# Kernel tuning notes

Hardware: AMD Instinct MI355X
Metric: run time of the kernel (lower is better)

## Reference

```python
import jax, jax.numpy as jnp
import numpy as np

N = 50000          # nodes
F = 128            # feature dim (indim = outdim)
AVG_DEG = 12       # random edges per node (plus one self-loop)
AVG_D_LOG = 2.6    # avg_d['log'] used by PNA scalers
EPS = 1e-5         # PNA std epsilon / BatchNorm eps


def setup_inputs() -> dict:
    key = jax.random.key(0)
    k1, k2, k3, k4 = jax.random.split(key, 4)
    h = jax.random.normal(k1, (N, F), dtype=jnp.float32)
    E_rand = N * AVG_DEG
    src_r = jax.random.randint(k2, (E_rand,), 0, N)
    dst_r = jax.random.randint(k3, (E_rand,), 0, N)
    loop = jnp.arange(N)
    src = jnp.concatenate([src_r, loop]).astype(jnp.int64) if jax.config.jax_enable_x64 else jnp.concatenate([src_r, loop]).astype(jnp.int32)
    dst = jnp.concatenate([dst_r, loop]).astype(src.dtype)
    concat_dim = F * (1 + 4 * 3)  # indim * (1 + n_aggr * n_scalers)
    W = jax.random.normal(k4, (concat_dim, F), dtype=jnp.float32) * (1.0 / np.sqrt(concat_dim))
    b = jnp.zeros((F,), dtype=jnp.float32)
    gamma = jnp.ones((F,), dtype=jnp.float32)
    beta = jnp.zeros((F,), dtype=jnp.float32)
    return {"h": h, "src": src, "dst": dst, "W": W, "b": b, "gamma": gamma, "beta": beta}


def _pna_forward(h, W, b, gamma, beta, src, dst):
    n = h.shape[0]
    m = h[src]                                            # [E, F] gathered mailbox
    deg = jax.ops.segment_sum(jnp.ones(src.shape[0], h.dtype), dst, num_segments=n)
    deg = jnp.maximum(deg, 1.0)[:, None]                  # every node has a self-loop
    s = jax.ops.segment_sum(m, dst, num_segments=n)
    mean = s / deg
    mx = jax.ops.segment_max(m, dst, num_segments=n)
    mn = jax.ops.segment_min(m, dst, num_segments=n)
    mean_sq = jax.ops.segment_sum(m * m, dst, num_segments=n) / deg
    std = jnp.sqrt(jax.nn.relu(mean_sq - mean * mean) + EPS)
    agg = jnp.concatenate([mean, mx, mn, std], axis=1)    # [N, 4F]
    logd = jnp.log(deg + 1.0)                             # [N, 1]
    scaled = jnp.concatenate([agg,
                              agg * (logd / AVG_D_LOG),
                              agg * (AVG_D_LOG / logd)], axis=1)  # [N, 12F]
    hc = jnp.concatenate([h, scaled], axis=1)             # [N, 13F]
    out = hc @ W + b                                      # posttrans (single linear)
    out = jax.nn.relu(out)                                # activation (dropout p=0)
    mu = out.mean(axis=0)                                 # BatchNorm1d, training stats
    var = out.var(axis=0)                                 # biased variance (torch)
    out = gamma * (out - mu) * jax.lax.rsqrt(var + EPS) + beta
    return out


def reference(h, src, dst, W, b, gamma, beta):
    return _pna_forward(h, W, b, gamma, beta, src, dst)
```

## Files before the change

kernel.cpp:

```cpp
#include <hip/hip_runtime.h>
#include <math.h>

#define FDIM 128
#define AVG_D_LOGF 2.6f
#define BN_EPS 1e-5f
#define NK 10

using f32x4 = __attribute__((ext_vector_type(4))) float;
using s16x8 = __attribute__((ext_vector_type(8))) short;
using u16x8 = __attribute__((ext_vector_type(8))) unsigned short;

__device__ __forceinline__ unsigned short f2bf(float x) {
  unsigned int u = __float_as_uint(x);
  u += 0x7FFFu + ((u >> 16) & 1u);
  return (unsigned short)(u >> 16);
}
__device__ __forceinline__ float bf2f(unsigned short u) {
  return __uint_as_float(((unsigned int)u) << 16);
}

__device__ __forceinline__ void gload16(const void* g, void* l) {
  __builtin_amdgcn_global_load_lds(
      (const __attribute__((address_space(1))) void*)g,
      (__attribute__((address_space(3))) void*)l, 16, 0, 0);
}

__global__ void prep_kernel(const float* __restrict__ h, unsigned short* __restrict__ hb,
                            const float* __restrict__ W, unsigned short* __restrict__ wBT,
                            const int* __restrict__ dst, int* __restrict__ deg,
                            int w0, int w1, int w2, int K) {
  int i = blockIdx.x * 256 + threadIdx.x;
  if (i < w0) {
    const f32x4* sp = (const f32x4*)h + (size_t)i * 2;
    f32x4 v0 = sp[0], v1 = sp[1];
    u16x8 o;
    o[0] = f2bf(v0[0]); o[1] = f2bf(v0[1]); o[2] = f2bf(v0[2]); o[3] = f2bf(v0[3]);
    o[4] = f2bf(v1[0]); o[5] = f2bf(v1[1]); o[6] = f2bf(v1[2]); o[7] = f2bf(v1[3]);
    *((u16x8*)hb + i) = o;
  } else if (i < w0 + w1) {
    int idx = i - w0;
    int k = idx >> 7, j = idx & 127;
    wBT[(size_t)j * K + k] = f2bf(W[idx]);
  } else if (i < w0 + w1 + w2) {
    atomicAdd(&deg[dst[i - w0 - w1]], 1);
  }
}

__global__ void scan1(const int* __restrict__ deg, int* __restrict__ offs,
                      int* __restrict__ bsums, int n) {
  __shared__ int tmp[256];
  int t = threadIdx.x, i = blockIdx.x * 256 + t;
  int v = (i < n) ? deg[i] : 0;
  tmp[t] = v; __syncthreads();
  for (int d = 1; d < 256; d <<= 1) {
    int x = (t >= d) ? tmp[t - d] : 0;
    __syncthreads();
    tmp[t] += x;
    __syncthreads();
  }
  if (i < n) offs[i] = tmp[t] - v;
  if (t == 255) bsums[blockIdx.x] = tmp[255];
}

__global__ void scan2(int* __restrict__ bsums, int nb) {
  __shared__ int tmp[256];
  int t = threadIdx.x;
  int v = (t < nb) ? bsums[t] : 0;
  tmp[t] = v; __syncthreads();
  for (int d = 1; d < 256; d <<= 1) {
    int x = (t >= d) ? tmp[t - d] : 0;
    __syncthreads();
    tmp[t] += x;
    __syncthreads();
  }
  if (t < nb) bsums[t] = tmp[t] - v;
}

__global__ void scan3(int* __restrict__ offs, const int* __restrict__ bsums, int n, int E) {
  int i = blockIdx.x * 256 + threadIdx.x;
  if (i < n) offs[i] += bsums[blockIdx.x];
  if (i == 0) offs[n] = E;
}

__global__ void csr_fill(const int* __restrict__ src, const int* __restrict__ dst,
                         const int* __restrict__ offs, int* __restrict__ cursor,
                         int* __restrict__ csr, int E) {
  int i = blockIdx.x * 256 + threadIdx.x;
  if (i < E) {
    int d = dst[i];
    int pos = offs[d] + atomicAdd(&cursor[d], 1);
    csr[pos] = src[i];
  }
}

__global__ __launch_bounds__(256) void agg_kernel(
    const unsigned short* __restrict__ hb, const int* __restrict__ csr,
    const int* __restrict__ offs, unsigned short* __restrict__ aggb,
    float2* __restrict__ s12a, int n) {
  const int gw = (blockIdx.x * 256 + threadIdx.x) >> 6;
  const int lane = threadIdx.x & 63;
  if (gw >= n) return;
  const int beg = offs[gw], end = offs[gw + 1];
  const unsigned int* hp = (const unsigned int*)hb;
  float s0 = 0.f, s1 = 0.f, q0 = 0.f, q1 = 0.f;
  float mx0 = -INFINITY, mx1 = -INFINITY, mn0 = INFINITY, mn1 = INFINITY;
  int e = beg;
  for (; e + 4 <= end; e += 4) {
    int i0 = csr[e], i1 = csr[e + 1], i2 = csr[e + 2], i3 = csr[e + 3];
    unsigned int a = hp[(size_t)i0 * 64 + lane];
    unsigned int b = hp[(size_t)i1 * 64 + lane];
    unsigned int c = hp[(size_t)i2 * 64 + lane];
    unsigned int d = hp[(size_t)i3 * 64 + lane];
    float a0 = bf2f((unsigned short)a), a1 = bf2f((unsigned short)(a >> 16));
    float b0 = bf2f((unsigned short)b), b1 = bf2f((unsigned short)(b >> 16));
    float c0 = bf2f((unsigned short)c), c1 = bf2f((unsigned short)(c >> 16));
    float d0 = bf2f((unsigned short)d), d1 = bf2f((unsigned short)(d >> 16));
    s0 += (a0 + b0) + (c0 + d0); s1 += (a1 + b1) + (c1 + d1);
    q0 += (a0 * a0 + b0 * b0) + (c0 * c0 + d0 * d0);
    q1 += (a1 * a1 + b1 * b1) + (c1 * c1 + d1 * d1);
    mx0 = fmaxf(fmaxf(mx0, a0), fmaxf(b0, fmaxf(c0, d0)));
    mx1 = fmaxf(fmaxf(mx1, a1), fmaxf(b1, fmaxf(c1, d1)));
    mn0 = fminf(fminf(mn0, a0), fminf(b0, fminf(c0, d0)));
    mn1 = fminf(fminf(mn1, a1), fminf(b1, fminf(c1, d1)));
  }
  for (; e < end; ++e) {
    int i0 = csr[e];
    unsigned int a = hp[(size_t)i0 * 64 + lane];
    float a0 = bf2f((unsigned short)a), a1 = bf2f((unsigned short)(a >> 16));
    s0 += a0; s1 += a1;
    q0 += a0 * a0; q1 += a1 * a1;
    mx0 = fmaxf(mx0, a0); mx1 = fmaxf(mx1, a1);
    mn0 = fminf(mn0, a0); mn1 = fminf(mn1, a1);
  }
  float degf = (float)(end - beg);
  if (degf < 1.f) degf = 1.f;
  const float inv = 1.f / degf;
  float me0 = s0 * inv, me1 = s1 * inv;
  float v0 = q0 * inv - me0 * me0, v1 = q1 * inv - me1 * me1;
  float st0 = sqrtf(fmaxf(v0, 0.f) + BN_EPS);
  float st1 = sqrtf(fmaxf(v1, 0.f) + BN_EPS);
  unsigned int base = (unsigned int)gw * 512u + (unsigned int)lane * 2u;
  *(unsigned int*)&aggb[base      ] = (unsigned int)f2bf(me0) | ((unsigned int)f2bf(me1) << 16);
  *(unsigned int*)&aggb[base + 128] = (unsigned int)f2bf(mx0) | ((unsigned int)f2bf(mx1) << 16);
  *(unsigned int*)&aggb[base + 256] = (unsigned int)f2bf(mn0) | ((unsigned int)f2bf(mn1) << 16);
  *(unsigned int*)&aggb[base + 384] = (unsigned int)f2bf(st0) | ((unsigned int)f2bf(st1) << 16);
  if (lane == 0) {
    float logd = logf(degf + 1.f);
    s12a[gw] = make_float2(logd / AVG_D_LOGF, AVG_D_LOGF / logd);
  }
}

__global__ __launch_bounds__(256, 3) void gemm_kernel(
    const unsigned short* __restrict__ hb, const unsigned short* __restrict__ wBT,
    const unsigned short* __restrict__ aggb, const float2* __restrict__ s12a,
    const float* __restrict__ bias, float* __restrict__ out,
    float* __restrict__ bnsum, float* __restrict__ bnsq, int n, int K) {
  __shared__ s16x8 As[1024];
  __shared__ s16x8 Bs[3][512];
  const int t = threadIdx.x;
  const int lane = t & 63;
  const int w = t >> 6;
  const int wr = w >> 1, wc = w & 1;
  const int hi = lane >> 4, lr = lane & 15, rx7 = lr & 7;

  const int nwg = gridDim.x;
  const int q = nwg >> 3, r = nwg & 7;
  const int xcd = blockIdx.x & 7, jj = blockIdx.x >> 3;
  const int bx = (xcd < r ? xcd * (q + 1) : r * (q + 1) + (xcd - r) * q) + jj;

  const int m0 = (bx >> 1) * 128;
  const int n0 = (bx & 1) * 64;

  f32x4 acc[3][4][2] = {};

  auto stage = [&](int ss) {
    const bool ph1 = (ss < 2);
    #pragma unroll
    for (int i = 0; i < 4; ++i) {
      int unit = w * 256 + i * 64 + lane;
      int row = unit >> 3, x = unit & 7;
      int node = m0 + row; if (node >= n) node = n - 1;
      int xo = (x ^ (row & 7)) << 3;
      const unsigned short* src = ph1
          ? hb   + (size_t)node * FDIM + ss * 64 + xo
          : aggb + (size_t)node * 512 + (ss - 2) * 64 + xo;
      gload16(src, &As[w * 256 + i * 64]);
    }
    const int nsec = ph1 ? 1 : 3;
    for (int s = 0; s < nsec; ++s) {
      int koff = ph1 ? ss * 64 : (FDIM + s * 512 + (ss - 2) * 64);
      #pragma unroll
      for (int i = 0; i < 2; ++i) {
        int unit = w * 128 + i * 64 + lane;
        int row = unit >> 3, x = unit & 7;
        const unsigned short* src =
            wBT + (size_t)(n0 + row) * K + koff + ((x ^ (row & 7)) << 3);
        gload16(src, &Bs[s][w * 128 + i * 64]);
      }
    }
  };

  for (int step = 0; step < NK; ++step) {
    stage(step);
    __syncthreads();
    #pragma unroll
    for (int ks = 0; ks < 2; ++ks) {
      s16x8 a[4];
      #pragma unroll
      for (int m = 0; m < 4; ++m) {
        int row = wr * 64 + m * 16 + lr;
        a[m] = As[row * 8 + ((ks * 4 + hi) ^ rx7)];
      }
      #pragma unroll
      for (int s = 0; s < 3; ++s) {
        if (step < 2 && s > 0) continue;
        int rb = wc * 32 + lr;
        s16x8 b0 = Bs[s][rb * 8 + ((ks * 4 + hi) ^ rx7)];
        s16x8 b1 = Bs[s][(rb + 16) * 8 + ((ks * 4 + hi) ^ rx7)];
        #pragma unroll
        for (int m = 0; m < 4; ++m) {
          acc[s][m][0] = __builtin_amdgcn_mfma_f32_16x16x32_bf16(a[m], b0, acc[s][m][0], 0, 0, 0);
          acc[s][m][1] = __builtin_amdgcn_mfma_f32_16x16x32_bf16(a[m], b1, acc[s][m][1], 0, 0, 0);
        }
      }
    }
    __syncthreads();
  }

  float* red = (float*)&As[0];
  if (t < 128) red[t] = 0.f;
  __syncthreads();

  const float bv0 = bias[n0 + wc * 32 + lr];
  const float bv1 = bias[n0 + wc * 32 + 16 + lr];
  float cs[2] = {0.f, 0.f}, cq[2] = {0.f, 0.f};
  #pragma unroll
  for (int m = 0; m < 4; ++m) {
    #pragma unroll
    for (int i = 0; i < 4; ++i) {
      int grow = m0 + wr * 64 + m * 16 + hi * 4 + i;
      if (grow >= n) continue;
      float2 sv = s12a[grow];
      #pragma unroll
      for (int nn = 0; nn < 2; ++nn) {
        float v = acc[0][m][nn][i] + sv.x * acc[1][m][nn][i] + sv.y * acc[2][m][nn][i]
                + (nn ? bv1 : bv0);
        v = fmaxf(v, 0.f);
        out[(size_t)grow * FDIM + n0 + wc * 32 + nn * 16 + lr] = v;
        cs[nn] += v; cq[nn] += v * v;
      }
    }
  }
  #pragma unroll
  for (int nn = 0; nn < 2; ++nn) {
    int lc = wc * 32 + nn * 16 + lr;
    atomicAdd(&red[lc], cs[nn]);
    atomicAdd(&red[64 + lc], cq[nn]);
  }
  __syncthreads();
  if (t < 64)       atomicAdd(&bnsum[n0 + t], red[t]);
  else if (t < 128) atomicAdd(&bnsq[n0 + t - 64], red[t]);
}

__global__ void bn_norm(float* __restrict__ out, const float* __restrict__ bnsum,
                        const float* __restrict__ bnsq, const float* __restrict__ gamma,
                        const float* __restrict__ beta, int n) {
  const int j = threadIdx.x & 127;
  const float invN = 1.f / (float)n;
  const float mu = bnsum[j] * invN;
  const float var = bnsq[j] * invN - mu * mu;
  const float rs = rsqrtf(var + BN_EPS);
  const float sc = gamma[j] * rs;
  const float sh = beta[j] - mu * sc;
  const int gt = blockIdx.x * 256 + threadIdx.x;
  const int row0 = gt >> 7;
  const int rstride = (gridDim.x * 256) >> 7;
  for (int i = row0; i < n; i += rstride) {
    size_t idx = (size_t)i * FDIM + j;
    out[idx] = out[idx] * sc + sh;
  }
}

extern "C" void kernel_launch(void* const* d_in, const int* in_sizes, int n_in,
                              void* d_out, int out_size, void* d_ws, size_t ws_size,
                              hipStream_t stream) {
  const float* h     = (const float*)d_in[0];
  const int*   src   = (const int*)d_in[1];
  const int*   dst   = (const int*)d_in[2];
  const float* W     = (const float*)d_in[3];
  const float* bias  = (const float*)d_in[4];
  const float* gamma = (const float*)d_in[5];
  const float* beta  = (const float*)d_in[6];
  float* out = (float*)d_out;

  const int n = in_sizes[0] / FDIM;
  const int E = in_sizes[1];
  const int K = in_sizes[3] / FDIM;

  char* base = (char*)d_ws;
  size_t off = 0;
  auto alloc = [&](size_t bytes) -> void* {
    void* p = base + off;
    off += (bytes + 255) & ~(size_t)255;
    return p;
  };
  int*   deg    = (int*)  alloc(4ull * n);
  int*   cursor = (int*)  alloc(4ull * n);
  float* bnsum  = (float*)alloc(512);
  float* bnsq   = (float*)alloc(512);
  const size_t zlen = off;
  int*    offs  = (int*)  alloc(4ull * (n + 1));
  int*    bsums = (int*)  alloc(4ull * 256);
  int*    csr   = (int*)  alloc(4ull * E);
  float2* s12a  = (float2*)alloc(8ull * n);
  unsigned short* aggb = (unsigned short*)alloc(2ull * (size_t)n * 512);
  unsigned short* wBT  = (unsigned short*)alloc(2ull * (size_t)K * FDIM);
  unsigned short* hb   = (unsigned short*)alloc(2ull * (size_t)n * FDIM);
  (void)ws_size; (void)n_in; (void)out_size;

  const int eb = (E + 255) / 256;
  const int nb = (n + 255) / 256;
  const int w0 = n * FDIM / 8;
  const int w1 = K * FDIM;
  const int w2 = E;

  hipMemsetAsync(d_ws, 0, zlen, stream);
  prep_kernel<<<(w0 + w1 + w2 + 255) / 256, 256, 0, stream>>>(h, hb, W, wBT, dst, deg,
                                                              w0, w1, w2, K);
  scan1<<<nb, 256, 0, stream>>>(deg, offs, bsums, n);
  scan2<<<1, 256, 0, stream>>>(bsums, nb);
  scan3<<<nb, 256, 0, stream>>>(offs, bsums, n, E);
  csr_fill<<<eb, 256, 0, stream>>>(src, dst, offs, cursor, csr, E);
  agg_kernel<<<(n + 3) / 4, 256, 0, stream>>>(hb, csr, offs, aggb, s12a, n);
  const int gblocks = ((n + 127) / 128) * 2;
  gemm_kernel<<<gblocks, 256, 0, stream>>>(hb, wBT, aggb, s12a, bias,
                                           out, bnsum, bnsq, n, K);
  bn_norm<<<1024, 256, 0, stream>>>(out, bnsum, bnsq, gamma, beta, n);
}
```

Measured before the change: 175.9 us.

## Drop LDS staging in GEMM and fold scan3 into consumers

The GEMM kernel no longer stages A and B tiles through LDS with global_load_lds and barriers. Each wave now loads its MFMA operands directly from global memory into registers, which removes the per-step __syncthreads and the LDS footprint. The third scan pass is also removed: csr_fill and agg_kernel add the block prefix sum from bsums when they read offsets. This saves a kernel launch, but operand reuse across waves now depends on L1/L2 caches instead of shared memory, so global load traffic and latency exposure rise.

Measured after the change: 226.0 us. 28.5% more time.

```diff
diff --git a/kernel.cpp b/kernel.cpp
--- a/kernel.cpp
+++ b/kernel.cpp
@@ -4,7 +4,6 @@
 #define FDIM 128
 #define AVG_D_LOGF 2.6f
 #define BN_EPS 1e-5f
-#define NK 10
 
 using f32x4 = __attribute__((ext_vector_type(4))) float;
 using s16x8 = __attribute__((ext_vector_type(8))) short;
@@ -17,12 +16,6 @@
 }
 __device__ __forceinline__ float bf2f(unsigned short u) {
   return __uint_as_float(((unsigned int)u) << 16);
-}
-
-__device__ __forceinline__ void gload16(const void* g, void* l) {
-  __builtin_amdgcn_global_load_lds(
-      (const __attribute__((address_space(1))) void*)g,
-      (__attribute__((address_space(3))) void*)l, 16, 0, 0);
 }
 
 __global__ void prep_kernel(const float* __restrict__ h, unsigned short* __restrict__ hb,
@@ -76,31 +69,26 @@
   if (t < nb) bsums[t] = tmp[t] - v;
 }
 
-__global__ void scan3(int* __restrict__ offs, const int* __restrict__ bsums, int n, int E) {
-  int i = blockIdx.x * 256 + threadIdx.x;
-  if (i < n) offs[i] += bsums[blockIdx.x];
-  if (i == 0) offs[n] = E;
-}
-
 __global__ void csr_fill(const int* __restrict__ src, const int* __restrict__ dst,
-                         const int* __restrict__ offs, int* __restrict__ cursor,
-                         int* __restrict__ csr, int E) {
+                         const int* __restrict__ offs, const int* __restrict__ bsums,
+                         int* __restrict__ cursor, int* __restrict__ csr, int E) {
   int i = blockIdx.x * 256 + threadIdx.x;
   if (i < E) {
     int d = dst[i];
-    int pos = offs[d] + atomicAdd(&cursor[d], 1);
+    int pos = offs[d] + bsums[d >> 8] + atomicAdd(&cursor[d], 1);
     csr[pos] = src[i];
   }
 }
 
 __global__ __launch_bounds__(256) void agg_kernel(
     const unsigned short* __restrict__ hb, const int* __restrict__ csr,
-    const int* __restrict__ offs, unsigned short* __restrict__ aggb,
-    float2* __restrict__ s12a, int n) {
+    const int* __restrict__ offs, const int* __restrict__ bsums,
+    unsigned short* __restrict__ aggb, float2* __restrict__ s12a, int n, int E) {
   const int gw = (blockIdx.x * 256 + threadIdx.x) >> 6;
   const int lane = threadIdx.x & 63;
   if (gw >= n) return;
-  const int beg = offs[gw], end = offs[gw + 1];
+  const int beg = offs[gw] + bsums[gw >> 8];
+  const int end = (gw + 1 < n) ? offs[gw + 1] + bsums[(gw + 1) >> 8] : E;
   const unsigned int* hp = (const unsigned int*)hb;
   float s0 = 0.f, s1 = 0.f, q0 = 0.f, q1 = 0.f;
   float mx0 = -INFINITY, mx1 = -INFINITY, mn0 = INFINITY, mn1 = INFINITY;
@@ -150,18 +138,17 @@
   }
 }
 
-__global__ __launch_bounds__(256, 3) void gemm_kernel(
+__global__ __launch_bounds__(256) void gemm_kernel(
     const unsigned short* __restrict__ hb, const unsigned short* __restrict__ wBT,
     const unsigned short* __restrict__ aggb, const float2* __restrict__ s12a,
     const float* __restrict__ bias, float* __restrict__ out,
     float* __restrict__ bnsum, float* __restrict__ bnsq, int n, int K) {
-  __shared__ s16x8 As[1024];
-  __shared__ s16x8 Bs[3][512];
+  __shared__ float red[128];
   const int t = threadIdx.x;
   const int lane = t & 63;
   const int w = t >> 6;
   const int wr = w >> 1, wc = w & 1;
-  const int hi = lane >> 4, lr = lane & 15, rx7 = lr & 7;
+  const int hi = lane >> 4, lr = lane & 15;
 
   const int nwg = gridDim.x;
   const int q = nwg >> 3, r = nwg & 7;
@@ -173,61 +160,68 @@
 
   f32x4 acc[3][4][2] = {};
 
-  auto stage = [&](int ss) {
-    const bool ph1 = (ss < 2);
-    #pragma unroll
-    for (int i = 0; i < 4; ++i) {
-      int unit = w * 256 + i * 64 + lane;
-      int row = unit >> 3, x = unit & 7;
-      int node = m0 + row; if (node >= n) node = n - 1;
-      int xo = (x ^ (row & 7)) << 3;
-      const unsigned short* src = ph1
-          ? hb   + (size_t)node * FDIM + ss * 64 + xo
-          : aggb + (size_t)node * 512 + (ss - 2) * 64 + xo;
-      gload16(src, &As[w * 256 + i * 64]);
+  const unsigned short* aH[4];
+  const unsigned short* aG[4];
+  #pragma unroll
+  for (int m = 0; m < 4; ++m) {
+    int row = m0 + wr * 64 + m * 16 + lr;
+    if (row >= n) row = n - 1;
+    aH[m] = hb   + (size_t)row * FDIM + hi * 8;
+    aG[m] = aggb + (size_t)row * 512  + hi * 8;
+  }
+  const unsigned short* bP[2];
+  #pragma unroll
+  for (int nn = 0; nn < 2; ++nn)
+    bP[nn] = wBT + (size_t)(n0 + wc * 32 + nn * 16 + lr) * K + hi * 8;
+
+  #pragma unroll
+  for (int step = 0; step < 2; ++step) {
+    const int kg = step * 64;
+    s16x8 a[2][4], b[2][2];
+    #pragma unroll
+    for (int ks = 0; ks < 2; ++ks) {
+      #pragma unroll
+      for (int m = 0; m < 4; ++m) a[ks][m] = *(const s16x8*)(aH[m] + kg + ks * 32);
+      #pragma unroll
+      for (int nn = 0; nn < 2; ++nn) b[ks][nn] = *(const s16x8*)(bP[nn] + kg + ks * 32);
     }
-    const int nsec = ph1 ? 1 : 3;
-    for (int s = 0; s < nsec; ++s) {
-      int koff = ph1 ? ss * 64 : (FDIM + s * 512 + (ss - 2) * 64);
-      #pragma unroll
-      for (int i = 0; i < 2; ++i) {
-        int unit = w * 128 + i * 64 + lane;
-        int row = unit >> 3, x = unit & 7;
-        const unsigned short* src =
-            wBT + (size_t)(n0 + row) * K + koff + ((x ^ (row & 7)) << 3);
-        gload16(src, &Bs[s][w * 128 + i * 64]);
-      }
+    #pragma unroll
+    for (int ks = 0; ks < 2; ++ks)
+      #pragma unroll
+      for (int m = 0; m < 4; ++m)
+        #pragma unroll
+        for (int nn = 0; nn < 2; ++nn)
+          acc[0][m][nn] = __builtin_amdgcn_mfma_f32_16x16x32_bf16(a[ks][m], b[ks][nn],
+                                                                  acc[0][m][nn], 0, 0, 0);
+  }
+
+  for (int step = 0; step < 8; ++step) {
+    const int kg = step * 64;
+    s16x8 a[2][4];
+    #pragma unroll
+    for (int ks = 0; ks < 2; ++ks)
+      #pragma unroll
+      for (int m = 0; m < 4; ++m) a[ks][m] = *(const s16x8*)(aG[m] + kg + ks * 32);
+    #pragma unroll
+    for (int s = 0; s < 3; ++s) {
+      const int koff = FDIM + s * 512 + kg;
+      s16x8 b[2][2];
+      #pragma unroll
+      for (int ks = 0; ks < 2; ++ks)
+        #pragma unroll
+        for (int nn = 0; nn < 2; ++nn)
+          b[ks][nn] = *(const s16x8*)(bP[nn] + koff + ks * 32);
+      #pragma unroll
+      for (int ks = 0; ks < 2; ++ks)
+        #pragma unroll
+        for (int m = 0; m < 4; ++m)
+          #pragma unroll
+          for (int nn = 0; nn < 2; ++nn)
+            acc[s][m][nn] = __builtin_amdgcn_mfma_f32_16x16x32_bf16(a[ks][m], b[ks][nn],
+                                                                    acc[s][m][nn], 0, 0, 0);
     }
-  };
-
-  for (int step = 0; step < NK; ++step) {
-    stage(step);
-    __syncthreads();
-    #pragma unroll
-    for (int ks = 0; ks < 2; ++ks) {
-      s16x8 a[4];
-      #pragma unroll
-      for (int m = 0; m < 4; ++m) {
-        int row = wr * 64 + m * 16 + lr;
-        a[m] = As[row * 8 + ((ks * 4 + hi) ^ rx7)];
-      }
-      #pragma unroll
-      for (int s = 0; s < 3; ++s) {
-        if (step < 2 && s > 0) continue;
-        int rb = wc * 32 + lr;
-        s16x8 b0 = Bs[s][rb * 8 + ((ks * 4 + hi) ^ rx7)];
-        s16x8 b1 = Bs[s][(rb + 16) * 8 + ((ks * 4 + hi) ^ rx7)];
-        #pragma unroll
-        for (int m = 0; m < 4; ++m) {
-          acc[s][m][0] = __builtin_amdgcn_mfma_f32_16x16x32_bf16(a[m], b0, acc[s][m][0], 0, 0, 0);
-          acc[s][m][1] = __builtin_amdgcn_mfma_f32_16x16x32_bf16(a[m], b1, acc[s][m][1], 0, 0, 0);
-        }
-      }
-    }
-    __syncthreads();
-  }
-
-  float* red = (float*)&As[0];
+  }
+
   if (t < 128) red[t] = 0.f;
   __syncthreads();
 
@@ -329,9 +323,8 @@
                                                               w0, w1, w2, K);
   scan1<<<nb, 256, 0, stream>>>(deg, offs, bsums, n);
   scan2<<<1, 256, 0, stream>>>(bsums, nb);
-  scan3<<<nb, 256, 0, stream>>>(offs, bsums, n, E);
-  csr_fill<<<eb, 256, 0, stream>>>(src, dst, offs, cursor, csr, E);
-  agg_kernel<<<(n + 3) / 4, 256, 0, stream>>>(hb, csr, offs, aggb, s12a, n);
+  csr_fill<<<eb, 256, 0, stream>>>(src, dst, offs, bsums, cursor, csr, E);
+  agg_kernel<<<(n + 3) / 4, 256, 0, stream>>>(hb, csr, offs, bsums, aggb, s12a, n, E);
   const int gblocks = ((n + 127) / 128) * 2;
   gemm_kernel<<<gblocks, 256, 0, stream>>>(hb, wBT, aggb, s12a, bias,
                                            out, bnsum, bnsq, n, K);
```

## Fold block-sum scan into consumers and split edges across half-waves in aggregation

Applied to the files above, without the earlier changes.

Removes the scan2/scan3 launches by having csr_fill and agg_kernel each redo the small block-sum prefix scan in shared memory and add it to the partial offsets. The aggregation kernel now has each half-wave handle alternate edges with 8-byte loads per lane, then combines the halves with cross-lane shuffles before writing. This cuts two launches and doubles the gathers in flight per edge step, at the cost of repeating the block-sum scan in every block and adding shuffle reductions.

New measurement: 184.1 us. 4.7% more time.

```diff
diff --git a/kernel.cpp b/kernel.cpp
--- a/kernel.cpp
+++ b/kernel.cpp
@@ -62,88 +62,127 @@
   if (t == 255) bsums[blockIdx.x] = tmp[255];
 }
 
-__global__ void scan2(int* __restrict__ bsums, int nb) {
+__global__ void csr_fill(const int* __restrict__ src, const int* __restrict__ dst,
+                         const int* __restrict__ offs, const int* __restrict__ bsums,
+                         int* __restrict__ cursor, int* __restrict__ csr, int E, int nb) {
   __shared__ int tmp[256];
-  int t = threadIdx.x;
-  int v = (t < nb) ? bsums[t] : 0;
-  tmp[t] = v; __syncthreads();
-  for (int d = 1; d < 256; d <<= 1) {
-    int x = (t >= d) ? tmp[t - d] : 0;
-    __syncthreads();
-    tmp[t] += x;
-    __syncthreads();
-  }
-  if (t < nb) bsums[t] = tmp[t] - v;
-}
-
-__global__ void scan3(int* __restrict__ offs, const int* __restrict__ bsums, int n, int E) {
-  int i = blockIdx.x * 256 + threadIdx.x;
-  if (i < n) offs[i] += bsums[blockIdx.x];
-  if (i == 0) offs[n] = E;
-}
-
-__global__ void csr_fill(const int* __restrict__ src, const int* __restrict__ dst,
-                         const int* __restrict__ offs, int* __restrict__ cursor,
-                         int* __restrict__ csr, int E) {
-  int i = blockIdx.x * 256 + threadIdx.x;
+  __shared__ int ex[256];
+  const int t = threadIdx.x;
+  {
+    int v = (t < nb) ? bsums[t] : 0;
+    tmp[t] = v; __syncthreads();
+    for (int d = 1; d < 256; d <<= 1) {
+      int x = (t >= d) ? tmp[t - d] : 0;
+      __syncthreads();
+      tmp[t] += x;
+      __syncthreads();
+    }
+    ex[t] = tmp[t] - v;
+    __syncthreads();
+  }
+  int i = blockIdx.x * 256 + t;
   if (i < E) {
     int d = dst[i];
-    int pos = offs[d] + atomicAdd(&cursor[d], 1);
+    int pos = offs[d] + ex[d >> 8] + atomicAdd(&cursor[d], 1);
     csr[pos] = src[i];
   }
 }
 
 __global__ __launch_bounds__(256) void agg_kernel(
     const unsigned short* __restrict__ hb, const int* __restrict__ csr,
-    const int* __restrict__ offs, unsigned short* __restrict__ aggb,
-    float2* __restrict__ s12a, int n) {
+    const int* __restrict__ offs, const int* __restrict__ bsums,
+    unsigned short* __restrict__ aggb, float2* __restrict__ s12a,
+    int n, int E, int nb) {
+  __shared__ int tmp[256];
+  __shared__ int ex[256];
+  {
+    int t = threadIdx.x;
+    int v = (t < nb) ? bsums[t] : 0;
+    tmp[t] = v; __syncthreads();
+    for (int d = 1; d < 256; d <<= 1) {
+      int x = (t >= d) ? tmp[t - d] : 0;
+      __syncthreads();
+      tmp[t] += x;
+      __syncthreads();
+    }
+    ex[t] = tmp[t] - v;
+    __syncthreads();
+  }
   const int gw = (blockIdx.x * 256 + threadIdx.x) >> 6;
   const int lane = threadIdx.x & 63;
   if (gw >= n) return;
-  const int beg = offs[gw], end = offs[gw + 1];
-  const unsigned int* hp = (const unsigned int*)hb;
-  float s0 = 0.f, s1 = 0.f, q0 = 0.f, q1 = 0.f;
-  float mx0 = -INFINITY, mx1 = -INFINITY, mn0 = INFINITY, mn1 = INFINITY;
-  int e = beg;
-  for (; e + 4 <= end; e += 4) {
-    int i0 = csr[e], i1 = csr[e + 1], i2 = csr[e + 2], i3 = csr[e + 3];
-    unsigned int a = hp[(size_t)i0 * 64 + lane];
-    unsigned int b = hp[(size_t)i1 * 64 + lane];
-    unsigned int c = hp[(size_t)i2 * 64 + lane];
-    unsigned int d = hp[(size_t)i3 * 64 + lane];
-    float a0 = bf2f((unsigned short)a), a1 = bf2f((unsigned short)(a >> 16));
-    float b0 = bf2f((unsigned short)b), b1 = bf2f((unsigned short)(b >> 16));
-    float c0 = bf2f((unsigned short)c), c1 = bf2f((unsigned short)(c >> 16));
-    float d0 = bf2f((unsigned short)d), d1 = bf2f((unsigned short)(d >> 16));
-    s0 += (a0 + b0) + (c0 + d0); s1 += (a1 + b1) + (c1 + d1);
-    q0 += (a0 * a0 + b0 * b0) + (c0 * c0 + d0 * d0);
-    q1 += (a1 * a1 + b1 * b1) + (c1 * c1 + d1 * d1);
-    mx0 = fmaxf(fmaxf(mx0, a0), fmaxf(b0, fmaxf(c0, d0)));
-    mx1 = fmaxf(fmaxf(mx1, a1), fmaxf(b1, fmaxf(c1, d1)));
-    mn0 = fminf(fminf(mn0, a0), fminf(b0, fminf(c0, d0)));
-    mn1 = fminf(fminf(mn1, a1), fminf(b1, fminf(c1, d1)));
-  }
-  for (; e < end; ++e) {
-    int i0 = csr[e];
-    unsigned int a = hp[(size_t)i0 * 64 + lane];
-    float a0 = bf2f((unsigned short)a), a1 = bf2f((unsigned short)(a >> 16));
-    s0 += a0; s1 += a1;
-    q0 += a0 * a0; q1 += a1 * a1;
-    mx0 = fmaxf(mx0, a0); mx1 = fmaxf(mx1, a1);
-    mn0 = fminf(mn0, a0); mn1 = fminf(mn1, a1);
-  }
-  float degf = (float)(end - beg);
+  const int beg = offs[gw] + ex[gw >> 8];
+  const int end = (gw + 1 < n) ? offs[gw + 1] + ex[(gw + 1) >> 8] : E;
+  const int sub = lane >> 5;
+  const int fl  = lane & 31;
+  const uint2* hp2 = (const uint2*)hb;
+
+  float s0=0.f,s1=0.f,s2=0.f,s3=0.f, q0=0.f,q1=0.f,q2=0.f,q3=0.f;
+  float mx0=-INFINITY,mx1=-INFINITY,mx2=-INFINITY,mx3=-INFINITY;
+  float mn0=INFINITY,mn1=INFINITY,mn2=INFINITY,mn3=INFINITY;
+
+  auto acc1 = [&](uint2 A) {
+    float a0 = bf2f((unsigned short)A.x), a1 = bf2f((unsigned short)(A.x >> 16));
+    float a2 = bf2f((unsigned short)A.y), a3 = bf2f((unsigned short)(A.y >> 16));
+    s0 += a0; s1 += a1; s2 += a2; s3 += a3;
+    q0 += a0*a0; q1 += a1*a1; q2 += a2*a2; q3 += a3*a3;
+    mx0 = fmaxf(mx0,a0); mx1 = fmaxf(mx1,a1); mx2 = fmaxf(mx2,a2); mx3 = fmaxf(mx3,a3);
+    mn0 = fminf(mn0,a0); mn1 = fminf(mn1,a1); mn2 = fminf(mn2,a2); mn3 = fminf(mn3,a3);
+  };
+
+  const int cnt = end - beg;
+  const int pairs = cnt >> 1;
+  int p = 0;
+  for (; p + 4 <= pairs; p += 4) {
+    int base = beg + 2 * p + sub;
+    int i0 = csr[base], i1 = csr[base + 2], i2 = csr[base + 4], i3 = csr[base + 6];
+    uint2 A = hp2[(size_t)i0 * 32 + fl];
+    uint2 B = hp2[(size_t)i1 * 32 + fl];
+    uint2 C = hp2[(size_t)i2 * 32 + fl];
+    uint2 D = hp2[(size_t)i3 * 32 + fl];
+    acc1(A); acc1(B); acc1(C); acc1(D);
+  }
+  for (; p < pairs; ++p) {
+    int i0 = csr[beg + 2 * p + sub];
+    acc1(hp2[(size_t)i0 * 32 + fl]);
+  }
+  if ((cnt & 1) && sub == 0) {
+    int i0 = csr[end - 1];
+    acc1(hp2[(size_t)i0 * 32 + fl]);
+  }
+
+  s0 += __shfl_xor(s0, 32); s1 += __shfl_xor(s1, 32);
+  s2 += __shfl_xor(s2, 32); s3 += __shfl_xor(s3, 32);
+  q0 += __shfl_xor(q0, 32); q1 += __shfl_xor(q1, 32);
+  q2 += __shfl_xor(q2, 32); q3 += __shfl_xor(q3, 32);
+  mx0 = fmaxf(mx0, __shfl_xor(mx0, 32)); mx1 = fmaxf(mx1, __shfl_xor(mx1, 32));
+  mx2 = fmaxf(mx2, __shfl_xor(mx2, 32)); mx3 = fmaxf(mx3, __shfl_xor(mx3, 32));
+  mn0 = fminf(mn0, __shfl_xor(mn0, 32)); mn1 = fminf(mn1, __shfl_xor(mn1, 32));
+  mn2 = fminf(mn2, __shfl_xor(mn2, 32)); mn3 = fminf(mn3, __shfl_xor(mn3, 32));
+
+  float degf = (float)cnt;
   if (degf < 1.f) degf = 1.f;
   const float inv = 1.f / degf;
-  float me0 = s0 * inv, me1 = s1 * inv;
-  float v0 = q0 * inv - me0 * me0, v1 = q1 * inv - me1 * me1;
-  float st0 = sqrtf(fmaxf(v0, 0.f) + BN_EPS);
-  float st1 = sqrtf(fmaxf(v1, 0.f) + BN_EPS);
-  unsigned int base = (unsigned int)gw * 512u + (unsigned int)lane * 2u;
-  *(unsigned int*)&aggb[base      ] = (unsigned int)f2bf(me0) | ((unsigned int)f2bf(me1) << 16);
-  *(unsigned int*)&aggb[base + 128] = (unsigned int)f2bf(mx0) | ((unsigned int)f2bf(mx1) << 16);
-  *(unsigned int*)&aggb[base + 256] = (unsigned int)f2bf(mn0) | ((unsigned int)f2bf(mn1) << 16);
-  *(unsigned int*)&aggb[base + 384] = (unsigned int)f2bf(st0) | ((unsigned int)f2bf(st1) << 16);
+  if (sub == 0) {
+    float me0 = s0*inv, me1 = s1*inv, me2 = s2*inv, me3 = s3*inv;
+    float st0 = sqrtf(fmaxf(q0*inv - me0*me0, 0.f) + BN_EPS);
+    float st1 = sqrtf(fmaxf(q1*inv - me1*me1, 0.f) + BN_EPS);
+    float st2 = sqrtf(fmaxf(q2*inv - me2*me2, 0.f) + BN_EPS);
+    float st3 = sqrtf(fmaxf(q3*inv - me3*me3, 0.f) + BN_EPS);
+    unsigned int b = (unsigned int)gw * 512u + (unsigned int)fl * 4u;
+    uint2 wme = make_uint2((unsigned int)f2bf(me0) | ((unsigned int)f2bf(me1) << 16),
+                           (unsigned int)f2bf(me2) | ((unsigned int)f2bf(me3) << 16));
+    uint2 wmx = make_uint2((unsigned int)f2bf(mx0) | ((unsigned int)f2bf(mx1) << 16),
+                           (unsigned int)f2bf(mx2) | ((unsigned int)f2bf(mx3) << 16));
+    uint2 wmn = make_uint2((unsigned int)f2bf(mn0) | ((unsigned int)f2bf(mn1) << 16),
+                           (unsigned int)f2bf(mn2) | ((unsigned int)f2bf(mn3) << 16));
+    uint2 wst = make_uint2((unsigned int)f2bf(st0) | ((unsigned int)f2bf(st1) << 16),
+                           (unsigned int)f2bf(st2) | ((unsigned int)f2bf(st3) << 16));
+    *(uint2*)&aggb[b      ] = wme;
+    *(uint2*)&aggb[b + 128] = wmx;
+    *(uint2*)&aggb[b + 256] = wmn;
+    *(uint2*)&aggb[b + 384] = wst;
+  }
   if (lane == 0) {
     float logd = logf(degf + 1.f);
     s12a[gw] = make_float2(logd / AVG_D_LOGF, AVG_D_LOGF / logd);
@@ -328,10 +367,8 @@
   prep_kernel<<<(w0 + w1 + w2 + 255) / 256, 256, 0, stream>>>(h, hb, W, wBT, dst, deg,
                                                               w0, w1, w2, K);
   scan1<<<nb, 256, 0, stream>>>(deg, offs, bsums, n);
-  scan2<<<1, 256, 0, stream>>>(bsums, nb);
-  scan3<<<nb, 256, 0, stream>>>(offs, bsums, n, E);
-  csr_fill<<<eb, 256, 0, stream>>>(src, dst, offs, cursor, csr, E);
-  agg_kernel<<<(n + 3) / 4, 256, 0, stream>>>(hb, csr, offs, aggb, s12a, n);
+  csr_fill<<<eb, 256, 0, stream>>>(src, dst, offs, bsums, cursor, csr, E, nb);
+  agg_kernel<<<(n + 3) / 4, 256, 0, stream>>>(hb, csr, offs, bsums, aggb, s12a, n, E, nb);
   const int gblocks = ((n + 127) / 128) * 2;
   gemm_kernel<<<gblocks, 256, 0, stream>>>(hb, wBT, aggb, s12a, bias,
                                            out, bnsum, bnsq, n, K);
```
